# Optimization experiments

Measured on AMD Instinct MI355X. Metric: run time of the kernel, lower is better.

Reference implementation:

```python
import jax, jax.numpy as jnp
import numpy as np


def setup_inputs() -> dict:
    key = jax.random.key(0)
    ks = jax.random.split(key, 8)
    B, T, D = 128, 2048, 100  # T <= 3000 (pos_emb table size)
    return {
        "h": jax.random.normal(ks[0], (B, T, D), jnp.float32),
        "d": jax.random.normal(ks[1], (B, 1, D), jnp.float32),
        # tf.random_normal_initializer default stddev = 0.05
        "w_c": 0.05 * jax.random.normal(ks[2], (D, 1), jnp.float32),
        "w_s": 0.05 * jax.random.normal(ks[3], (D, D), jnp.float32),
        "w_r": 0.05 * jax.random.normal(ks[4], (D, D), jnp.float32),
        "pos_table": 0.05 * jax.random.normal(ks[5], (3000, D), jnp.float32),
        "w_ap": 0.05 * jax.random.normal(ks[6], (D, 1), jnp.float32),
        "b": jnp.zeros((1,), jnp.float32),
    }


def reference(h, d, w_c, w_s, w_r, pos_table, w_ap, b):
    # h: [B, T, D]   d: [B, 1, D]   D == 100
    B, T, D = h.shape
    content = jnp.einsum('btd,dk->bt', h, w_c)              # [B, T]
    ds = jnp.einsum('bod,de->boe', d, w_s)[:, 0]            # [B, D]
    salience = jnp.einsum('btd,bd->bt', h, ds)              # [B, T]
    abs_pos = (pos_table[:T] @ w_ap)[:, 0]                  # [T]
    pre = content + salience + abs_pos[None, :] + b[0]      # [B, T]

    # At j == 0 the original skips the state update (s stays zero) and uses
    # no novelty term; tanh(0) @ w_r == 0 so the uniform formula matches p_0.
    mask = (jnp.arange(T) > 0).astype(h.dtype)              # [T]

    def step(s, x):
        h_j, pre_j, m = x                                   # [B,D], [B], []
        nov = jnp.sum(h_j * (jnp.tanh(s) @ w_r), axis=-1)   # [B]
        p = jax.nn.sigmoid(pre_j - nov)                     # [B]
        s = s + h_j * (p * m)[:, None]                      # accumulate state
        return s, p

    s0 = jnp.zeros((B, D), h.dtype)
    _, P = jax.lax.scan(step, s0, (jnp.swapaxes(h, 0, 1), pre.T, mask))
    return P.T  # [B, T] extraction probabilities
```

## Files before the change

### kernel.cpp

```cpp
#include <hip/hip_runtime.h>

#define D 100
#define TT 2048
#define BB 128
#define CHUNK 64
#define NCHUNK (TT / CHUNK)
#define NTHR 832

static __device__ __constant__ float KLO = 2.8853900817779268f;
static __device__ __constant__ float MKF = -2.8853900817779268f;

#define DPP_ADD(q, ctrl)                                                      \
  q += __int_as_float(__builtin_amdgcn_update_dpp(                            \
      0, __float_as_int(q), ctrl, 0xF, 0xF, true))

__global__ void k1_pos(const float* __restrict__ pos, const float* __restrict__ wap,
                       const float* __restrict__ bb, float* __restrict__ ab2m) {
  int j = blockIdx.x * blockDim.x + threadIdx.x;
  if (j < TT) {
    float a = 0.f;
    #pragma unroll 4
    for (int e = 0; e < D; ++e) a = fmaf(pos[j * D + e], wap[e], a);
    ab2m[j] = -1.4426950408889634f * (a + bb[0]);
  }
}

template <int NQ>
__device__ __forceinline__ float prod_dot(const float* wr, const float4* hr) {
  float a0 = 0.f, a1 = 0.f;
  #pragma unroll
  for (int qd = 0; qd < NQ; ++qd) {
    const float4 hv = hr[qd];
    a0 = fmaf(hv.x, wr[4 * qd + 0], a0);
    a1 = fmaf(hv.y, wr[4 * qd + 1], a1);
    a0 = fmaf(hv.z, wr[4 * qd + 2], a0);
    a1 = fmaf(hv.w, wr[4 * qd + 3], a1);
  }
  return a0 + a1;
}

__global__ void __launch_bounds__(NTHR)
sp_scan(const float* __restrict__ h, const float* __restrict__ dv,
        const float* __restrict__ w_c, const float* __restrict__ w_s,
        const float* __restrict__ w_r, const float* __restrict__ ab2m,
        float* __restrict__ out) {
  __shared__ float gbuf[2][CHUNK][256];
  __shared__ float crow_s[128];
  const int b = blockIdx.x;
  const int tid = (int)threadIdx.x;
  const int lane = tid & 63;
  const int wvu = __builtin_amdgcn_readfirstlane(tid) >> 6;

  const int q = wvu - 1;
  const int grp = q >> 2;
  const int blk = (q & 3) >> 1;
  const int hf = q & 1;
  const int eoff = hf ? 52 : 0;
  const int col = hf * 128 + blk * 64 + lane;

  if (tid < 128) {
    float acc = 0.f;
    if (tid < D) {
      float a1 = 0.f, a2 = 0.f;
      for (int dd = 0; dd < D; ++dd) {
        a1 = fmaf(dv[b * D + dd], w_s[dd * D + tid], a1);
        a2 += w_r[dd * D + tid];
      }
      acc = w_c[tid] + a1 - a2;
    }
    crow_s[tid] = acc;
  }
  __syncthreads();

  float wr[52];
  if (wvu != 0) {
    const int row = blk * 64 + lane;
    if (row < D) {
      const float* src = w_r + row * D + eoff;
      if (hf == 0) {
        #pragma unroll
        for (int e = 0; e < 52; ++e) wr[e] = src[e];
      } else {
        #pragma unroll
        for (int e = 0; e < 48; ++e) wr[e] = src[e];
        wr[48] = wr[49] = wr[50] = wr[51] = 0.f;
      }
    } else if (row == D) {
      if (hf == 0) {
        #pragma unroll
        for (int e = 0; e < 52; ++e) wr[e] = crow_s[e];
      } else {
        #pragma unroll
        for (int e = 0; e < 48; ++e) wr[e] = crow_s[52 + e];
        wr[48] = wr[49] = wr[50] = wr[51] = 0.f;
      }
    } else {
      #pragma unroll
      for (int e = 0; e < 52; ++e) wr[e] = 0.f;
    }
  }

  const float* hb = h + (size_t)b * TT * D;

  float Slo = 0.f, Shi = 0.f, c = 0.f, hlp = 0.f, hhp = 0.f, pout = 0.f;
  float hlb[8], hhb[8], abb[8];

  if (wvu == 0) {
    __builtin_amdgcn_s_setprio(1);
    #pragma unroll
    for (int i = 0; i < 8; ++i) {
      float sc = (i == 0) ? 0.f : KLO;
      hlb[i] = sc * hb[(size_t)i * D + lane];
      hhb[i] = (lane < 36) ? sc * hb[(size_t)i * D + lane + 64] : 0.f;
      abb[i] = ab2m[i];
    }
  } else {
    for (int s = grp; s < CHUNK; s += 3) {
      const float* hrow = hb + (size_t)s * D + eoff;
      float v;
      if (hf == 0) v = prod_dot<13>(wr, (const float4*)hrow);
      else         v = prod_dot<12>(wr, (const float4*)hrow);
      gbuf[0][s][col] = v;
    }
  }
  __syncthreads();

  for (int cc = 0; cc < NCHUNK; ++cc) {
    if (wvu == 0) {
      float(*gb)[256] = gbuf[cc & 1];
      float g0l = gb[0][lane] + gb[0][128 + lane];
      float g0h = gb[0][64 + lane] + gb[0][192 + lane];
      float g1l = gb[1][lane] + gb[1][128 + lane];
      float g1h = gb[1][64 + lane] + gb[1][192 + lane];
      #pragma unroll 8
      for (int s = 0; s < CHUNK; ++s) {
        const int j = cc * CHUNK + s;
        float hlv = hlb[s & 7], hhv = hhb[s & 7], abv = abb[s & 7];
        {
          int jn = j + 8;
          if (jn >= TT) jn = TT - 1;
          const size_t off = (size_t)jn * D;
          hlb[s & 7] = KLO * hb[off + lane];
          hhb[s & 7] = (lane < 36) ? KLO * hb[off + lane + 64] : 0.f;
          abb[s & 7] = ab2m[jn];
        }
        float g2l = 0.f, g2h = 0.f;
        if (s < CHUNK - 2) {
          g2l = gb[s + 2][lane] + gb[s + 2][128 + lane];
          g2h = gb[s + 2][64 + lane] + gb[s + 2][192 + lane];
        }

        Slo = fmaf(hlp, c, Slo);
        Shi = fmaf(hhp, c, Shi);
        float rlo = __builtin_amdgcn_rcpf(1.f + __builtin_amdgcn_exp2f(Slo));
        float rhi = __builtin_amdgcn_rcpf(1.f + __builtin_amdgcn_exp2f(Shi));
        float qq = rlo * g0l;
        qq = fmaf(rhi, g0h, qq);
        DPP_ADD(qq, 0xB1);
        DPP_ADD(qq, 0x4E);
        DPP_ADD(qq, 0x141);
        DPP_ADD(qq, 0x140);
        const int qi = __float_as_int(qq);
        float ra = __int_as_float(__builtin_amdgcn_readlane(qi, 0)) +
                   __int_as_float(__builtin_amdgcn_readlane(qi, 16));
        float rb = __int_as_float(__builtin_amdgcn_readlane(qi, 32)) +
                   __int_as_float(__builtin_amdgcn_readlane(qi, 48));
        float R = ra + rb;
        float nz = fmaf(MKF, R, abv);
        float p = __builtin_amdgcn_rcpf(1.f + __builtin_amdgcn_exp2f(nz));
        pout = (lane == s) ? p : pout;
        c = p;
        hlp = hlv;
        hhp = hhv;
        g0l = g1l; g0h = g1h; g1l = g2l; g1h = g2h;
      }
      out[(size_t)b * TT + cc * CHUNK + lane] = pout;
    } else if (cc + 1 < NCHUNK) {
      float(*gw)[256] = gbuf[(cc + 1) & 1];
      const int jbase = (cc + 1) * CHUNK;
      for (int s = grp; s < CHUNK; s += 3) {
        const float* hrow = hb + (size_t)(jbase + s) * D + eoff;
        float v;
        if (hf == 0) v = prod_dot<13>(wr, (const float4*)hrow);
        else         v = prod_dot<12>(wr, (const float4*)hrow);
        gw[s][col] = v;
      }
    }
    __syncthreads();
  }
}

extern "C" void kernel_launch(void* const* d_in, const int* in_sizes, int n_in,
                              void* d_out, int out_size, void* d_ws, size_t ws_size,
                              hipStream_t stream) {
  const float* h   = (const float*)d_in[0];
  const float* dv  = (const float*)d_in[1];
  const float* w_c = (const float*)d_in[2];
  const float* w_s = (const float*)d_in[3];
  const float* w_r = (const float*)d_in[4];
  const float* pos = (const float*)d_in[5];
  const float* wap = (const float*)d_in[6];
  const float* bb  = (const float*)d_in[7];
  float* out = (float*)d_out;
  float* ab2m = (float*)d_ws;

  hipLaunchKernelGGL(k1_pos, dim3(TT / 256), dim3(256), 0, stream, pos, wap, bb, ab2m);
  hipLaunchKernelGGL(sp_scan, dim3(BB), dim3(NTHR), 0, stream,
                     h, dv, w_c, w_s, w_r, ab2m, out);
}
```

Before: 552.6 us.

## Stage h chunks in LDS via dedicated loader wave, halve chunk size

Adds a 14th wave that copies h rows from global memory into a triple-buffered shared-memory stage two chunks ahead. Both the serial scan wave and the matvec waves then read h from LDS instead of global memory. This is meant to take global-load latency off the serial critical path. The chunk size is halved to 32 and the per-batch prologue vector is computed in parallel across five partial sums. The costs are twice as many block barriers and more shared memory use.

```diff
diff --git a/kernel.cpp b/kernel.cpp
--- a/kernel.cpp
+++ b/kernel.cpp
@@ -3,9 +3,9 @@
 #define D 100
 #define TT 2048
 #define BB 128
-#define CHUNK 64
+#define CHUNK 32
 #define NCHUNK (TT / CHUNK)
-#define NTHR 832
+#define NTHR 896
 
 static __device__ __constant__ float KLO = 2.8853900817779268f;
 static __device__ __constant__ float MKF = -2.8853900817779268f;
@@ -25,31 +25,41 @@
   }
 }
 
-template <int NQ>
-__device__ __forceinline__ float prod_dot(const float* wr, const float4* hr) {
-  float a0 = 0.f, a1 = 0.f;
-  #pragma unroll
-  for (int qd = 0; qd < NQ; ++qd) {
-    const float4 hv = hr[qd];
-    a0 = fmaf(hv.x, wr[4 * qd + 0], a0);
-    a1 = fmaf(hv.y, wr[4 * qd + 1], a1);
-    a0 = fmaf(hv.z, wr[4 * qd + 2], a0);
-    a1 = fmaf(hv.w, wr[4 * qd + 3], a1);
-  }
-  return a0 + a1;
-}
-
 __global__ void __launch_bounds__(NTHR)
 sp_scan(const float* __restrict__ h, const float* __restrict__ dv,
         const float* __restrict__ w_c, const float* __restrict__ w_s,
         const float* __restrict__ w_r, const float* __restrict__ ab2m,
         float* __restrict__ out) {
-  __shared__ float gbuf[2][CHUNK][256];
+  __shared__ __align__(16) float gbuf[2][CHUNK][256];
+  __shared__ __align__(16) float hstage[3][CHUNK][104];
   __shared__ float crow_s[128];
   const int b = blockIdx.x;
   const int tid = (int)threadIdx.x;
   const int lane = tid & 63;
   const int wvu = __builtin_amdgcn_readfirstlane(tid) >> 6;
+
+  const float* hb = h + (size_t)b * TT * D;
+
+  {
+    float* sc = &gbuf[0][0][0];
+    if (tid < 640) {
+      const int e = tid & 127;
+      const int part = tid >> 7;
+      float a1 = 0.f, a2 = 0.f;
+      if (e < D) {
+        const int d0 = part * 20;
+        #pragma unroll 4
+        for (int k = 0; k < 20; ++k) {
+          const float dvv = dv[b * D + d0 + k];
+          a1 = fmaf(dvv, w_s[(d0 + k) * D + e], a1);
+          a2 += w_r[(d0 + k) * D + e];
+        }
+      }
+      sc[part * 128 + e] = a1;
+      sc[640 + part * 128 + e] = a2;
+    }
+  }
+  __syncthreads();
 
   const int q = wvu - 1;
   const int grp = q >> 2;
@@ -57,99 +67,119 @@
   const int hf = q & 1;
   const int eoff = hf ? 52 : 0;
   const int col = hf * 128 + blk * 64 + lane;
+  const int row = blk * 64 + lane;
+
+  float wr[52];
 
   if (tid < 128) {
-    float acc = 0.f;
-    if (tid < D) {
-      float a1 = 0.f, a2 = 0.f;
-      for (int dd = 0; dd < D; ++dd) {
-        a1 = fmaf(dv[b * D + dd], w_s[dd * D + tid], a1);
-        a2 += w_r[dd * D + tid];
-      }
-      acc = w_c[tid] + a1 - a2;
-    }
-    crow_s[tid] = acc;
-  }
-  __syncthreads();
-
-  float wr[52];
-  if (wvu != 0) {
-    const int row = blk * 64 + lane;
+    const float* sc = &gbuf[0][0][0];
+    float a1 = sc[tid] + sc[128 + tid] + sc[256 + tid] + sc[384 + tid] + sc[512 + tid];
+    float a2 = sc[640 + tid] + sc[768 + tid] + sc[896 + tid] + sc[1024 + tid] + sc[1152 + tid];
+    crow_s[tid] = (tid < D) ? (w_c[tid] + a1 - a2) : 0.f;
+  }
+  if (wvu >= 1 && wvu <= 12) {
     if (row < D) {
-      const float* src = w_r + row * D + eoff;
+      const float4* src = (const float4*)(w_r + row * D + eoff);
       if (hf == 0) {
         #pragma unroll
-        for (int e = 0; e < 52; ++e) wr[e] = src[e];
+        for (int k = 0; k < 13; ++k) {
+          const float4 v = src[k];
+          wr[4*k] = v.x; wr[4*k+1] = v.y; wr[4*k+2] = v.z; wr[4*k+3] = v.w;
+        }
       } else {
         #pragma unroll
-        for (int e = 0; e < 48; ++e) wr[e] = src[e];
-        wr[48] = wr[49] = wr[50] = wr[51] = 0.f;
-      }
-    } else if (row == D) {
-      if (hf == 0) {
-        #pragma unroll
-        for (int e = 0; e < 52; ++e) wr[e] = crow_s[e];
-      } else {
-        #pragma unroll
-        for (int e = 0; e < 48; ++e) wr[e] = crow_s[52 + e];
+        for (int k = 0; k < 12; ++k) {
+          const float4 v = src[k];
+          wr[4*k] = v.x; wr[4*k+1] = v.y; wr[4*k+2] = v.z; wr[4*k+3] = v.w;
+        }
         wr[48] = wr[49] = wr[50] = wr[51] = 0.f;
       }
     } else {
       #pragma unroll
-      for (int e = 0; e < 52; ++e) wr[e] = 0.f;
-    }
-  }
-
-  const float* hb = h + (size_t)b * TT * D;
+      for (int k = 0; k < 52; ++k) wr[k] = 0.f;
+    }
+  } else if (wvu == 13) {
+    for (int s = 0; s < CHUNK; ++s) {
+      const float* hr = hb + (size_t)s * D;
+      hstage[0][s][lane] = hr[lane];
+      if (lane < 40) hstage[0][s][64 + lane] = (lane < 36) ? hr[64 + lane] : 0.f;
+    }
+  }
+  __syncthreads();
 
   float Slo = 0.f, Shi = 0.f, c = 0.f, hlp = 0.f, hhp = 0.f, pout = 0.f;
-  float hlb[8], hhb[8], abb[8];
+  float hlr0 = 0.f, hlr1 = 0.f, hhr0 = 0.f, hhr1 = 0.f, abrow_ = 0.f;
 
   if (wvu == 0) {
     __builtin_amdgcn_s_setprio(1);
-    #pragma unroll
-    for (int i = 0; i < 8; ++i) {
-      float sc = (i == 0) ? 0.f : KLO;
-      hlb[i] = sc * hb[(size_t)i * D + lane];
-      hhb[i] = (lane < 36) ? sc * hb[(size_t)i * D + lane + 64] : 0.f;
-      abb[i] = ab2m[i];
+    abrow_ = ab2m[lane & 31];
+    hlr0 = hstage[0][0][lane];
+    hlr1 = hstage[0][1][lane];
+    if (lane < 36) { hhr0 = hstage[0][0][64 + lane]; hhr1 = hstage[0][1][64 + lane]; }
+  } else if (wvu <= 12) {
+    if (row == D) {
+      const float* src = crow_s + eoff;
+      if (hf == 0) {
+        #pragma unroll
+        for (int k = 0; k < 52; ++k) wr[k] = src[k];
+      } else {
+        #pragma unroll
+        for (int k = 0; k < 48; ++k) wr[k] = src[k];
+        wr[48] = wr[49] = wr[50] = wr[51] = 0.f;
+      }
+    }
+    for (int s = grp; s < CHUNK; s += 3) {
+      const float4* hq = (const float4*)&hstage[0][s][eoff];
+      float a0 = 0.f, a1 = 0.f;
+      #pragma unroll
+      for (int k = 0; k < 13; ++k) {
+        const float4 v = hq[k];
+        a0 = fmaf(v.x, wr[4*k+0], a0);
+        a1 = fmaf(v.y, wr[4*k+1], a1);
+        a0 = fmaf(v.z, wr[4*k+2], a0);
+        a1 = fmaf(v.w, wr[4*k+3], a1);
+      }
+      gbuf[0][s][col] = a0 + a1;
     }
   } else {
-    for (int s = grp; s < CHUNK; s += 3) {
-      const float* hrow = hb + (size_t)s * D + eoff;
-      float v;
-      if (hf == 0) v = prod_dot<13>(wr, (const float4*)hrow);
-      else         v = prod_dot<12>(wr, (const float4*)hrow);
-      gbuf[0][s][col] = v;
+    const float* hc = hb + (size_t)CHUNK * D;
+    for (int s = 0; s < CHUNK; ++s) {
+      const float* hr = hc + (size_t)s * D;
+      hstage[1][s][lane] = hr[lane];
+      if (lane < 40) hstage[1][s][64 + lane] = (lane < 36) ? hr[64 + lane] : 0.f;
     }
   }
   __syncthreads();
 
+  int bufc = 0;
   for (int cc = 0; cc < NCHUNK; ++cc) {
+    const int bufn = (bufc == 2) ? 0 : bufc + 1;
     if (wvu == 0) {
-      float(*gb)[256] = gbuf[cc & 1];
+      float (*gb)[256] = gbuf[cc & 1];
       float g0l = gb[0][lane] + gb[0][128 + lane];
       float g0h = gb[0][64 + lane] + gb[0][192 + lane];
       float g1l = gb[1][lane] + gb[1][128 + lane];
       float g1h = gb[1][64 + lane] + gb[1][192 + lane];
-      #pragma unroll 8
+      const int ncc = (cc + 1 < NCHUNK) ? cc + 1 : cc;
+      float abn = ab2m[ncc * CHUNK + (lane & 31)];
+      const bool notlast = (cc != NCHUNK - 1);
+      #pragma unroll
       for (int s = 0; s < CHUNK; ++s) {
-        const int j = cc * CHUNK + s;
-        float hlv = hlb[s & 7], hhv = hhb[s & 7], abv = abb[s & 7];
-        {
-          int jn = j + 8;
-          if (jn >= TT) jn = TT - 1;
-          const size_t off = (size_t)jn * D;
-          hlb[s & 7] = KLO * hb[off + lane];
-          hhb[s & 7] = (lane < 36) ? KLO * hb[off + lane + 64] : 0.f;
-          abb[s & 7] = ab2m[jn];
+        float hlN = 0.f, hhN = 0.f;
+        if (s < CHUNK - 2) {
+          const float* hr = &hstage[bufc][s + 2][0];
+          hlN = hr[lane];
+          if (lane < 36) hhN = hr[64 + lane];
+        } else if (notlast) {
+          const float* hr = &hstage[bufn][s + 2 - CHUNK][0];
+          hlN = hr[lane];
+          if (lane < 36) hhN = hr[64 + lane];
         }
         float g2l = 0.f, g2h = 0.f;
         if (s < CHUNK - 2) {
           g2l = gb[s + 2][lane] + gb[s + 2][128 + lane];
           g2h = gb[s + 2][64 + lane] + gb[s + 2][192 + lane];
         }
-
         Slo = fmaf(hlp, c, Slo);
         Shi = fmaf(hhp, c, Shi);
         float rlo = __builtin_amdgcn_rcpf(1.f + __builtin_amdgcn_exp2f(Slo));
@@ -166,27 +196,54 @@
         float rb = __int_as_float(__builtin_amdgcn_readlane(qi, 32)) +
                    __int_as_float(__builtin_amdgcn_readlane(qi, 48));
         float R = ra + rb;
+        float abv = __int_as_float(
+            __builtin_amdgcn_readlane(__float_as_int(abrow_), s));
         float nz = fmaf(MKF, R, abv);
         float p = __builtin_amdgcn_rcpf(1.f + __builtin_amdgcn_exp2f(nz));
         pout = (lane == s) ? p : pout;
         c = p;
-        hlp = hlv;
-        hhp = hhv;
+        float hl_cur = (s & 1) ? hlr1 : hlr0;
+        float hh_cur = (s & 1) ? hhr1 : hhr0;
+        hlp = KLO * hl_cur;
+        hhp = KLO * hh_cur;
+        if (s == 0) {
+          if (cc == 0) { hlp = 0.f; hhp = 0.f; }
+        }
+        if (s & 1) { hlr1 = hlN; hhr1 = hhN; } else { hlr0 = hlN; hhr0 = hhN; }
         g0l = g1l; g0h = g1h; g1l = g2l; g1h = g2h;
       }
-      out[(size_t)b * TT + cc * CHUNK + lane] = pout;
-    } else if (cc + 1 < NCHUNK) {
-      float(*gw)[256] = gbuf[(cc + 1) & 1];
-      const int jbase = (cc + 1) * CHUNK;
-      for (int s = grp; s < CHUNK; s += 3) {
-        const float* hrow = hb + (size_t)(jbase + s) * D + eoff;
-        float v;
-        if (hf == 0) v = prod_dot<13>(wr, (const float4*)hrow);
-        else         v = prod_dot<12>(wr, (const float4*)hrow);
-        gw[s][col] = v;
+      if (lane < CHUNK) out[(size_t)b * TT + cc * CHUNK + lane] = pout;
+      abrow_ = abn;
+    } else if (wvu <= 12) {
+      if (cc + 1 < NCHUNK) {
+        float (*gw)[256] = gbuf[(cc + 1) & 1];
+        for (int s = grp; s < CHUNK; s += 3) {
+          const float4* hq = (const float4*)&hstage[bufn][s][eoff];
+          float a0 = 0.f, a1 = 0.f;
+          #pragma unroll
+          for (int k = 0; k < 13; ++k) {
+            const float4 v = hq[k];
+            a0 = fmaf(v.x, wr[4*k+0], a0);
+            a1 = fmaf(v.y, wr[4*k+1], a1);
+            a0 = fmaf(v.z, wr[4*k+2], a0);
+            a1 = fmaf(v.w, wr[4*k+3], a1);
+          }
+          gw[s][col] = a0 + a1;
+        }
+      }
+    } else {
+      if (cc + 2 < NCHUNK) {
+        const int bufs = (bufn == 2) ? 0 : bufn + 1;
+        const float* hc = hb + (size_t)(cc + 2) * CHUNK * D;
+        for (int s = 0; s < CHUNK; ++s) {
+          const float* hr = hc + (size_t)s * D;
+          hstage[bufs][s][lane] = hr[lane];
+          if (lane < 40) hstage[bufs][s][64 + lane] = (lane < 36) ? hr[64 + lane] : 0.f;
+        }
       }
     }
     __syncthreads();
+    bufc = bufn;
   }
 }
 
```

After: 1.816 ms. +228.6%, slower.
